# Optimization experiments

Measured on AMD Instinct MI355X. Metric: run time of the kernel, lower is better.

The kernel has to match this reference:

```python
import jax, jax.numpy as jnp
import numpy as np

B, S, P = 256, 1024, 4096   # batch, n_sensors, n_points
NM, H, PD = 64, 128, 128    # n_modes, hidden width, p
C = 1.0                     # speed of light param


def setup_inputs() -> dict:
    key = jax.random.key(0)
    ks = jax.random.split(key, 16)
    w = lambda k, shp: (jax.random.normal(k, shp, jnp.float32) * 0.05)
    return {
        "u0": jax.random.normal(ks[0], (B, S), jnp.float32),
        "x": jax.random.uniform(ks[1], (P,), jnp.float32, -1.0, 1.0),
        "t": jax.random.uniform(ks[2], (P,), jnp.float32, 0.0, 1.0),
        # branch MLP: (2*NM)->128->128->PD
        "bw1": w(ks[3], (H, 2 * NM)), "bb1": jnp.zeros((H,), jnp.float32),
        "bw2": w(ks[4], (H, H)),      "bb2": jnp.zeros((H,), jnp.float32),
        "bw3": w(ks[5], (PD, H)),     "bb3": jnp.zeros((PD,), jnp.float32),
        # trunk MLP: 4->128->128->PD
        "tw1": w(ks[6], (H, 4)),      "tb1": jnp.zeros((H,), jnp.float32),
        "tw2": w(ks[7], (H, H)),      "tb2": jnp.zeros((H,), jnp.float32),
        "tw3": w(ks[8], (PD, H)),     "tb3": jnp.zeros((PD,), jnp.float32),
    }


def _mlp(a, w1, b1, w2, b2, w3, b3):
    a = jax.nn.relu(a @ w1.T + b1)
    a = jax.nn.relu(a @ w2.T + b2)
    return a @ w3.T + b3


def reference(u0, x, t, bw1, bb1, bw2, bb2, bw3, bb3, tw1, tb1, tw2, tb2, tw3, tb3):
    # Fourier coefficients: mean over sensors of u0 * cos/sin(pi*k*xs)
    xs = jnp.linspace(-1.0, 1.0, S, dtype=jnp.float32)          # (S,)
    modes = jnp.arange(1, NM + 1, dtype=jnp.float32)            # (NM,)
    ang = jnp.pi * modes[:, None] * xs[None, :]                 # (NM, S)
    cos_c = (u0 @ jnp.cos(ang).T) / S                           # (B, NM)
    sin_c = (u0 @ jnp.sin(ang).T) / S                           # (B, NM)
    fourier = jnp.concatenate([cos_c, sin_c], axis=1)           # (B, 2*NM)

    branch_out = _mlp(fourier, bw1, bb1, bw2, bb2, bw3, bb3)    # (B, PD)

    xe = jnp.broadcast_to(x[None, :], (u0.shape[0], P))         # (B, P)
    te = jnp.broadcast_to(t[None, :], (u0.shape[0], P))
    pt_sq = te ** 2 - xe ** 2 / (C ** 2)
    # safe sqrt of clamp(pt_sq, min=0)
    proper_time = jnp.sqrt(jnp.where(pt_sq > 0, pt_sq, 0.0) + 0.0)
    causal = (jnp.abs(xe) <= C * te).astype(jnp.float32)
    trunk_feat = jnp.stack([xe, te, proper_time, causal], axis=-1)  # (B, P, 4)

    trunk_out = _mlp(trunk_feat, tw1, tb1, tw2, tb2, tw3, tb3)      # (B, P, PD)

    u_pred = jnp.einsum("bd,bpd->bp", branch_out, trunk_out)        # (B, P)
    return u_pred * causal
```

## Files before the change

### kernel.cpp

```cpp
#include <hip/hip_runtime.h>
#include <hip/hip_fp16.h>
#include <math.h>

#define NMODES 64
#define SDIM   1024
#define BATCH  256
#define PDIM   4096
#define HDIM   128

typedef _Float16 half8 __attribute__((ext_vector_type(8)));
typedef float f32x4 __attribute__((ext_vector_type(4)));

#define WSB_BRANCH 0
#define WSB_T3     (BATCH * HDIM * 2)

__global__ __launch_bounds__(256) void k_fused(
    const float* __restrict__ u0,
    const float* __restrict__ xv, const float* __restrict__ tv,
    const float* __restrict__ bw1, const float* __restrict__ bb1,
    const float* __restrict__ bw2, const float* __restrict__ bb2,
    const float* __restrict__ bw3, const float* __restrict__ bb3,
    const float* __restrict__ tw1, const float* __restrict__ tb1,
    const float* __restrict__ tw2, const float* __restrict__ tb2,
    const float* __restrict__ tw3, const float* __restrict__ tb3,
    __half* __restrict__ branch_out, __half* __restrict__ t3g) {
    __shared__ float h1L[16 * 132];
    __shared__ float h2L[16 * 132];
    __shared__ float featL[16][4];
    __shared__ float u0s[2][SDIM];
    __shared__ float part[2][2][HDIM];
    __shared__ float fr[2][HDIM];
    __shared__ float hh[2][HDIM];

    const int t = threadIdx.x;

    if (blockIdx.x < 256) {
        const int pbase = blockIdx.x * 16;
        const int j = t & 127;
        const int pg = t >> 7;

        if (t < 16) {
            int p = pbase + t;
            float x = xv[p], tt = tv[p];
            float q = tt * tt - x * x;
            float ptime = (q > 0.f) ? sqrtf(q) : 0.f;
            float c = (fabsf(x) <= tt) ? 1.f : 0.f;
            featL[t][0] = x; featL[t][1] = tt; featL[t][2] = ptime; featL[t][3] = c;
        }
        __syncthreads();

        {
            float4 w1 = ((const float4*)tw1)[j];
            float b1 = tb1[j];
            for (int p = pg; p < 16; p += 2) {
                float4 f = *(const float4*)featL[p];
                float v = fmaf(w1.x, f.x, fmaf(w1.y, f.y, fmaf(w1.z, f.z, fmaf(w1.w, f.w, b1))));
                h1L[p * 132 + j] = fmaxf(v, 0.f);
            }
        }
        __syncthreads();

        {
            const float4* wp = (const float4*)(tw2 + (size_t)j * HDIM);
            float bias = tb2[j];
            float acc[8];
#pragma unroll
            for (int q = 0; q < 8; ++q) acc[q] = bias;
            for (int i4 = 0; i4 < 32; ++i4) {
                float4 wv = wp[i4];
#pragma unroll
                for (int q = 0; q < 8; ++q) {
                    float4 hv = *(const float4*)&h1L[(pg + q * 2) * 132 + i4 * 4];
                    acc[q] += wv.x * hv.x + wv.y * hv.y + wv.z * hv.z + wv.w * hv.w;
                }
            }
#pragma unroll
            for (int q = 0; q < 8; ++q) h2L[(pg + q * 2) * 132 + j] = fmaxf(acc[q], 0.f);
        }
        __syncthreads();

        {
            const float4* wp = (const float4*)(tw3 + (size_t)j * HDIM);
            float bias = tb3[j];
            float acc[8];
#pragma unroll
            for (int q = 0; q < 8; ++q) acc[q] = bias;
            for (int i4 = 0; i4 < 32; ++i4) {
                float4 wv = wp[i4];
#pragma unroll
                for (int q = 0; q < 8; ++q) {
                    float4 hv = *(const float4*)&h2L[(pg + q * 2) * 132 + i4 * 4];
                    acc[q] += wv.x * hv.x + wv.y * hv.y + wv.z * hv.z + wv.w * hv.w;
                }
            }
#pragma unroll
            for (int q = 0; q < 8; ++q)
                t3g[(size_t)(pbase + pg + q * 2) * HDIM + j] = __float2half(acc[q]);
        }
        return;
    }

    const int bb = (blockIdx.x - 256) * 2;
    const int j = t & 127;
    const int half = t >> 7;

    {
        int flat0 = t;
        int row0 = flat0 >> 8, c40 = flat0 & 255;
        ((float4*)u0s[row0])[c40] = ((const float4*)(u0 + (size_t)(bb + row0) * SDIM))[c40];
        int flat1 = t + 256;
        int row1 = flat1 >> 8, c41 = flat1 & 255;
        ((float4*)u0s[row1])[c41] = ((const float4*)(u0 + (size_t)(bb + row1) * SDIM))[c41];
    }
    __syncthreads();

    {
        const int kmode = (j & 63) + 1;
        const int s_lo = half * 512;
        float xs0 = -1.0f + 2.0f * (float)s_lo / 1023.0f;
        float a = 0.5f * (float)kmode * xs0;
        a = a - floorf(a);
        const float r = (float)kmode * (1.0f / 1023.0f);
        float a0 = 0.f, a1 = 0.f;
        if (j < 64) {
#pragma unroll 8
            for (int s = s_lo; s < s_lo + 512; ++s) {
                float bas = __builtin_amdgcn_cosf(a);
                a += r; a = a - floorf(a);
                a0 += bas * u0s[0][s];
                a1 += bas * u0s[1][s];
            }
        } else {
#pragma unroll 8
            for (int s = s_lo; s < s_lo + 512; ++s) {
                float bas = __builtin_amdgcn_sinf(a);
                a += r; a = a - floorf(a);
                a0 += bas * u0s[0][s];
                a1 += bas * u0s[1][s];
            }
        }
        part[half][0][j] = a0;
        part[half][1][j] = a1;
    }
    __syncthreads();
    if (t < 128) {
        const float sc = 1.0f / (float)SDIM;
        fr[0][j] = (part[0][0][j] + part[1][0][j]) * sc;
        fr[1][j] = (part[0][1][j] + part[1][1][j]) * sc;
    }
    __syncthreads();

    if (t < 128) {
        {
            const float4* wp = (const float4*)(bw1 + (size_t)j * HDIM);
            float c0 = bb1[j], c1 = c0;
            for (int i4 = 0; i4 < 32; ++i4) {
                float4 wv = wp[i4];
                float4 x0 = *(const float4*)&fr[0][i4 * 4];
                float4 x1 = *(const float4*)&fr[1][i4 * 4];
                c0 += wv.x * x0.x + wv.y * x0.y + wv.z * x0.z + wv.w * x0.w;
                c1 += wv.x * x1.x + wv.y * x1.y + wv.z * x1.z + wv.w * x1.w;
            }
            hh[0][j] = fmaxf(c0, 0.f); hh[1][j] = fmaxf(c1, 0.f);
        }
        __syncthreads();
        {
            const float4* wp = (const float4*)(bw2 + (size_t)j * HDIM);
            float c0 = bb2[j], c1 = c0;
            for (int i4 = 0; i4 < 32; ++i4) {
                float4 wv = wp[i4];
                float4 x0 = *(const float4*)&hh[0][i4 * 4];
                float4 x1 = *(const float4*)&hh[1][i4 * 4];
                c0 += wv.x * x0.x + wv.y * x0.y + wv.z * x0.z + wv.w * x0.w;
                c1 += wv.x * x1.x + wv.y * x1.y + wv.z * x1.z + wv.w * x1.w;
            }
            fr[0][j] = fmaxf(c0, 0.f); fr[1][j] = fmaxf(c1, 0.f);
        }
        __syncthreads();
        {
            const float4* wp = (const float4*)(bw3 + (size_t)j * HDIM);
            float c0 = bb3[j], c1 = c0;
            for (int i4 = 0; i4 < 32; ++i4) {
                float4 wv = wp[i4];
                float4 x0 = *(const float4*)&fr[0][i4 * 4];
                float4 x1 = *(const float4*)&fr[1][i4 * 4];
                c0 += wv.x * x0.x + wv.y * x0.y + wv.z * x0.z + wv.w * x0.w;
                c1 += wv.x * x1.x + wv.y * x1.y + wv.z * x1.z + wv.w * x1.w;
            }
            branch_out[(size_t)(bb + 0) * HDIM + j] = __float2half(c0);
            branch_out[(size_t)(bb + 1) * HDIM + j] = __float2half(c1);
        }
    } else {
        __syncthreads();
        __syncthreads();
    }
}

#define LDH 144
__global__ __launch_bounds__(256) void k_final(
    const __half* __restrict__ br_g, const __half* __restrict__ t3g,
    const float* __restrict__ xv, const float* __restrict__ tv,
    float* __restrict__ out) {
    __shared__ _Float16 brL[64 * LDH];
    __shared__ _Float16 ttL[64 * LDH];
    __shared__ float causL[64];

    const int t = threadIdx.x;
    const int rb = blockIdx.x >> 6;
    const int cb = blockIdx.x & 63;

    if (t < 64) {
        int p = cb * 64 + t;
        float x = xv[p], tt = tv[p];
        causL[t] = (fabsf(x) <= tt) ? 1.f : 0.f;
    }

#pragma unroll
    for (int it = 0; it < 4; ++it) {
        int flat = t + 256 * it;
        int row = flat >> 4, c = flat & 15;
        *(float4*)&brL[row * LDH + c * 8] =
            *(const float4*)&br_g[(size_t)(rb * 64 + row) * HDIM + c * 8];
        *(float4*)&ttL[row * LDH + c * 8] =
            *(const float4*)&t3g[(size_t)(cb * 64 + row) * HDIM + c * 8];
    }
    __syncthreads();

    const int lane = t & 63;
    const int w = t >> 6;
    const int lm = lane & 15;
    const int q = lane >> 4;

    f32x4 acc[4] = {f32x4{0,0,0,0}, f32x4{0,0,0,0}, f32x4{0,0,0,0}, f32x4{0,0,0,0}};

    const _Float16* aBase = &brL[(16 * w + lm) * LDH + q * 8];
#pragma unroll
    for (int ks = 0; ks < 4; ++ks) {
        half8 af = *(const half8*)(aBase + ks * 32);
#pragma unroll
        for (int jt = 0; jt < 4; ++jt) {
            half8 bf = *(const half8*)&ttL[(16 * jt + lm) * LDH + q * 8 + ks * 32];
            acc[jt] = __builtin_amdgcn_mfma_f32_16x16x32_f16(af, bf, acc[jt], 0, 0, 0);
        }
    }

#pragma unroll
    for (int jt = 0; jt < 4; ++jt) {
        int col = cb * 64 + 16 * jt + lm;
        float cz = causL[16 * jt + lm];
#pragma unroll
        for (int e = 0; e < 4; ++e) {
            int row = rb * 64 + 16 * w + q * 4 + e;
            out[(size_t)row * PDIM + col] = acc[jt][e] * cz;
        }
    }
}

extern "C" void kernel_launch(void* const* d_in, const int* in_sizes, int n_in,
                              void* d_out, int out_size, void* d_ws, size_t ws_size,
                              hipStream_t stream) {
    const float* u0  = (const float*)d_in[0];
    const float* xv  = (const float*)d_in[1];
    const float* tv  = (const float*)d_in[2];
    const float* bw1 = (const float*)d_in[3];
    const float* bb1 = (const float*)d_in[4];
    const float* bw2 = (const float*)d_in[5];
    const float* bb2 = (const float*)d_in[6];
    const float* bw3 = (const float*)d_in[7];
    const float* bb3 = (const float*)d_in[8];
    const float* tw1 = (const float*)d_in[9];
    const float* tb1 = (const float*)d_in[10];
    const float* tw2 = (const float*)d_in[11];
    const float* tb2 = (const float*)d_in[12];
    const float* tw3 = (const float*)d_in[13];
    const float* tb3 = (const float*)d_in[14];

    char* wsb = (char*)d_ws;
    __half* branch_out = (__half*)(wsb + WSB_BRANCH);
    __half* t3g        = (__half*)(wsb + WSB_T3);
    float* out = (float*)d_out;

    hipLaunchKernelGGL(k_fused, dim3(384), dim3(256), 0, stream,
                       u0, xv, tv, bw1, bb1, bw2, bb2, bw3, bb3,
                       tw1, tb1, tw2, tb2, tw3, tb3, branch_out, t3g);
    hipLaunchKernelGGL(k_final, dim3(256), dim3(256), 0, stream,
                       branch_out, t3g, xv, tv, out);
}
```

Baseline: 107.3 us.

## Merge both kernels into one cooperative launch with grid sync and even/odd folding

Fuses the trunk/branch MLP kernel and the final MFMA contraction into a single cooperative kernel of 256 blocks, separated by a grid-wide sync, with shared memory overlaid through a union. Each block now handles 16 trunk points plus one batch row of the branch path. The Fourier projection uses the symmetry of the sensor grid, folding u0 into even and odd halves so the cos and sin loops run over half as many samples. This removes a kernel launch and gap and balances work across blocks, at the cost of a grid barrier and lower per-block parallelism in the branch MLP.

```diff
diff --git a/kernel.cpp b/kernel.cpp
--- a/kernel.cpp
+++ b/kernel.cpp
@@ -1,12 +1,16 @@
 #include <hip/hip_runtime.h>
 #include <hip/hip_fp16.h>
+#include <hip/hip_cooperative_groups.h>
 #include <math.h>
+
+namespace cg = cooperative_groups;
 
 #define NMODES 64
 #define SDIM   1024
 #define BATCH  256
 #define PDIM   4096
 #define HDIM   128
+#define LDH    144
 
 typedef _Float16 half8 __attribute__((ext_vector_type(8)));
 typedef float f32x4 __attribute__((ext_vector_type(4)));
@@ -14,7 +18,24 @@
 #define WSB_BRANCH 0
 #define WSB_T3     (BATCH * HDIM * 2)
 
-__global__ __launch_bounds__(256) void k_fused(
+struct P1 {
+    float h1L[16 * 132];
+    float h2L[16 * 132];
+    float featL[16][4];
+    float ue[512];
+    float uo[512];
+    float part[2][HDIM];
+    float fr[HDIM];
+    float hh[HDIM];
+};
+struct P2 {
+    _Float16 brL[64 * LDH];
+    _Float16 ttL[64 * LDH];
+    float causL[64];
+};
+union SharedU { P1 p1; P2 p2; };
+
+__global__ __launch_bounds__(256) void k_all(
     const float* __restrict__ u0,
     const float* __restrict__ xv, const float* __restrict__ tv,
     const float* __restrict__ bw1, const float* __restrict__ bb1,
@@ -23,29 +44,25 @@
     const float* __restrict__ tw1, const float* __restrict__ tb1,
     const float* __restrict__ tw2, const float* __restrict__ tb2,
     const float* __restrict__ tw3, const float* __restrict__ tb3,
-    __half* __restrict__ branch_out, __half* __restrict__ t3g) {
-    __shared__ float h1L[16 * 132];
-    __shared__ float h2L[16 * 132];
-    __shared__ float featL[16][4];
-    __shared__ float u0s[2][SDIM];
-    __shared__ float part[2][2][HDIM];
-    __shared__ float fr[2][HDIM];
-    __shared__ float hh[2][HDIM];
+    __half* __restrict__ branch_out, __half* __restrict__ t3g,
+    float* __restrict__ out) {
+    __shared__ SharedU sh;
 
     const int t = threadIdx.x;
-
-    if (blockIdx.x < 256) {
-        const int pbase = blockIdx.x * 16;
-        const int j = t & 127;
-        const int pg = t >> 7;
-
+    const int b = blockIdx.x;
+    const int j = t & 127;
+    const int pg = t >> 7;
+
+    {
+        const int pbase = b * 16;
         if (t < 16) {
             int p = pbase + t;
             float x = xv[p], tt = tv[p];
             float q = tt * tt - x * x;
             float ptime = (q > 0.f) ? sqrtf(q) : 0.f;
             float c = (fabsf(x) <= tt) ? 1.f : 0.f;
-            featL[t][0] = x; featL[t][1] = tt; featL[t][2] = ptime; featL[t][3] = c;
+            sh.p1.featL[t][0] = x; sh.p1.featL[t][1] = tt;
+            sh.p1.featL[t][2] = ptime; sh.p1.featL[t][3] = c;
         }
         __syncthreads();
 
@@ -53,9 +70,9 @@
             float4 w1 = ((const float4*)tw1)[j];
             float b1 = tb1[j];
             for (int p = pg; p < 16; p += 2) {
-                float4 f = *(const float4*)featL[p];
+                float4 f = *(const float4*)sh.p1.featL[p];
                 float v = fmaf(w1.x, f.x, fmaf(w1.y, f.y, fmaf(w1.z, f.z, fmaf(w1.w, f.w, b1))));
-                h1L[p * 132 + j] = fmaxf(v, 0.f);
+                sh.p1.h1L[p * 132 + j] = fmaxf(v, 0.f);
             }
         }
         __syncthreads();
@@ -70,12 +87,12 @@
                 float4 wv = wp[i4];
 #pragma unroll
                 for (int q = 0; q < 8; ++q) {
-                    float4 hv = *(const float4*)&h1L[(pg + q * 2) * 132 + i4 * 4];
+                    float4 hv = *(const float4*)&sh.p1.h1L[(pg + q * 2) * 132 + i4 * 4];
                     acc[q] += wv.x * hv.x + wv.y * hv.y + wv.z * hv.z + wv.w * hv.w;
                 }
             }
 #pragma unroll
-            for (int q = 0; q < 8; ++q) h2L[(pg + q * 2) * 132 + j] = fmaxf(acc[q], 0.f);
+            for (int q = 0; q < 8; ++q) sh.p1.h2L[(pg + q * 2) * 132 + j] = fmaxf(acc[q], 0.f);
         }
         __syncthreads();
 
@@ -89,7 +106,7 @@
                 float4 wv = wp[i4];
 #pragma unroll
                 for (int q = 0; q < 8; ++q) {
-                    float4 hv = *(const float4*)&h2L[(pg + q * 2) * 132 + i4 * 4];
+                    float4 hv = *(const float4*)&sh.p1.h2L[(pg + q * 2) * 132 + i4 * 4];
                     acc[q] += wv.x * hv.x + wv.y * hv.y + wv.z * hv.z + wv.w * hv.w;
                 }
             }
@@ -97,161 +114,136 @@
             for (int q = 0; q < 8; ++q)
                 t3g[(size_t)(pbase + pg + q * 2) * HDIM + j] = __float2half(acc[q]);
         }
-        return;
-    }
-
-    const int bb = (blockIdx.x - 256) * 2;
-    const int j = t & 127;
-    const int half = t >> 7;
-
-    {
-        int flat0 = t;
-        int row0 = flat0 >> 8, c40 = flat0 & 255;
-        ((float4*)u0s[row0])[c40] = ((const float4*)(u0 + (size_t)(bb + row0) * SDIM))[c40];
-        int flat1 = t + 256;
-        int row1 = flat1 >> 8, c41 = flat1 & 255;
-        ((float4*)u0s[row1])[c41] = ((const float4*)(u0 + (size_t)(bb + row1) * SDIM))[c41];
     }
     __syncthreads();
 
     {
-        const int kmode = (j & 63) + 1;
-        const int s_lo = half * 512;
-        float xs0 = -1.0f + 2.0f * (float)s_lo / 1023.0f;
-        float a = 0.5f * (float)kmode * xs0;
-        a = a - floorf(a);
-        const float r = (float)kmode * (1.0f / 1023.0f);
-        float a0 = 0.f, a1 = 0.f;
-        if (j < 64) {
+        const float* up = u0 + (size_t)b * SDIM;
+        for (int s = t; s < 512; s += 256) {
+            float a = up[s];
+            float c = up[1023 - s];
+            sh.p1.ue[s] = a + c;
+            sh.p1.uo[s] = a - c;
+        }
+        __syncthreads();
+
+        {
+            const int kmode = (j & 63) + 1;
+            const int s_lo = pg * 256;
+            float a = 0.5f * (float)kmode * (-1.0f + 2.0f * (float)s_lo / 1023.0f);
+            a -= floorf(a);
+            const float r = (float)kmode * (1.0f / 1023.0f);
+            float acc = 0.f;
+            if (j < 64) {
 #pragma unroll 8
-            for (int s = s_lo; s < s_lo + 512; ++s) {
-                float bas = __builtin_amdgcn_cosf(a);
-                a += r; a = a - floorf(a);
-                a0 += bas * u0s[0][s];
-                a1 += bas * u0s[1][s];
-            }
-        } else {
+                for (int s = s_lo; s < s_lo + 256; ++s) {
+                    float bas = __builtin_amdgcn_cosf(a);
+                    a += r; a -= floorf(a);
+                    acc += bas * sh.p1.ue[s];
+                }
+            } else {
 #pragma unroll 8
-            for (int s = s_lo; s < s_lo + 512; ++s) {
-                float bas = __builtin_amdgcn_sinf(a);
-                a += r; a = a - floorf(a);
-                a0 += bas * u0s[0][s];
-                a1 += bas * u0s[1][s];
-            }
-        }
-        part[half][0][j] = a0;
-        part[half][1][j] = a1;
+                for (int s = s_lo; s < s_lo + 256; ++s) {
+                    float bas = __builtin_amdgcn_sinf(a);
+                    a += r; a -= floorf(a);
+                    acc += bas * sh.p1.uo[s];
+                }
+            }
+            sh.p1.part[pg][j] = acc;
+        }
+        __syncthreads();
+        if (t < 128)
+            sh.p1.fr[j] = (sh.p1.part[0][j] + sh.p1.part[1][j]) * (1.0f / (float)SDIM);
+        __syncthreads();
+
+        float c0 = 0.f;
+        if (t < 128) {
+            const float4* wp = (const float4*)(bw1 + (size_t)j * HDIM);
+            c0 = bb1[j];
+            for (int i4 = 0; i4 < 32; ++i4) {
+                float4 wv = wp[i4];
+                float4 x0 = *(const float4*)&sh.p1.fr[i4 * 4];
+                c0 += wv.x * x0.x + wv.y * x0.y + wv.z * x0.z + wv.w * x0.w;
+            }
+        }
+        __syncthreads();
+        if (t < 128) sh.p1.hh[j] = fmaxf(c0, 0.f);
+        __syncthreads();
+        if (t < 128) {
+            const float4* wp = (const float4*)(bw2 + (size_t)j * HDIM);
+            c0 = bb2[j];
+            for (int i4 = 0; i4 < 32; ++i4) {
+                float4 wv = wp[i4];
+                float4 x0 = *(const float4*)&sh.p1.hh[i4 * 4];
+                c0 += wv.x * x0.x + wv.y * x0.y + wv.z * x0.z + wv.w * x0.w;
+            }
+        }
+        __syncthreads();
+        if (t < 128) sh.p1.fr[j] = fmaxf(c0, 0.f);
+        __syncthreads();
+        if (t < 128) {
+            const float4* wp = (const float4*)(bw3 + (size_t)j * HDIM);
+            c0 = bb3[j];
+            for (int i4 = 0; i4 < 32; ++i4) {
+                float4 wv = wp[i4];
+                float4 x0 = *(const float4*)&sh.p1.fr[i4 * 4];
+                c0 += wv.x * x0.x + wv.y * x0.y + wv.z * x0.z + wv.w * x0.w;
+            }
+            branch_out[(size_t)b * HDIM + j] = __float2half(c0);
+        }
     }
-    __syncthreads();
-    if (t < 128) {
-        const float sc = 1.0f / (float)SDIM;
-        fr[0][j] = (part[0][0][j] + part[1][0][j]) * sc;
-        fr[1][j] = (part[0][1][j] + part[1][1][j]) * sc;
-    }
-    __syncthreads();
-
-    if (t < 128) {
-        {
-            const float4* wp = (const float4*)(bw1 + (size_t)j * HDIM);
-            float c0 = bb1[j], c1 = c0;
-            for (int i4 = 0; i4 < 32; ++i4) {
-                float4 wv = wp[i4];
-                float4 x0 = *(const float4*)&fr[0][i4 * 4];
-                float4 x1 = *(const float4*)&fr[1][i4 * 4];
-                c0 += wv.x * x0.x + wv.y * x0.y + wv.z * x0.z + wv.w * x0.w;
-                c1 += wv.x * x1.x + wv.y * x1.y + wv.z * x1.z + wv.w * x1.w;
-            }
-            hh[0][j] = fmaxf(c0, 0.f); hh[1][j] = fmaxf(c1, 0.f);
-        }
-        __syncthreads();
-        {
-            const float4* wp = (const float4*)(bw2 + (size_t)j * HDIM);
-            float c0 = bb2[j], c1 = c0;
-            for (int i4 = 0; i4 < 32; ++i4) {
-                float4 wv = wp[i4];
-                float4 x0 = *(const float4*)&hh[0][i4 * 4];
-                float4 x1 = *(const float4*)&hh[1][i4 * 4];
-                c0 += wv.x * x0.x + wv.y * x0.y + wv.z * x0.z + wv.w * x0.w;
-                c1 += wv.x * x1.x + wv.y * x1.y + wv.z * x1.z + wv.w * x1.w;
-            }
-            fr[0][j] = fmaxf(c0, 0.f); fr[1][j] = fmaxf(c1, 0.f);
-        }
-        __syncthreads();
-        {
-            const float4* wp = (const float4*)(bw3 + (size_t)j * HDIM);
-            float c0 = bb3[j], c1 = c0;
-            for (int i4 = 0; i4 < 32; ++i4) {
-                float4 wv = wp[i4];
-                float4 x0 = *(const float4*)&fr[0][i4 * 4];
-                float4 x1 = *(const float4*)&fr[1][i4 * 4];
-                c0 += wv.x * x0.x + wv.y * x0.y + wv.z * x0.z + wv.w * x0.w;
-                c1 += wv.x * x1.x + wv.y * x1.y + wv.z * x1.z + wv.w * x1.w;
-            }
-            branch_out[(size_t)(bb + 0) * HDIM + j] = __float2half(c0);
-            branch_out[(size_t)(bb + 1) * HDIM + j] = __float2half(c1);
-        }
-    } else {
-        __syncthreads();
-        __syncthreads();
-    }
-}
-
-#define LDH 144
-__global__ __launch_bounds__(256) void k_final(
-    const __half* __restrict__ br_g, const __half* __restrict__ t3g,
-    const float* __restrict__ xv, const float* __restrict__ tv,
-    float* __restrict__ out) {
-    __shared__ _Float16 brL[64 * LDH];
-    __shared__ _Float16 ttL[64 * LDH];
-    __shared__ float causL[64];
-
-    const int t = threadIdx.x;
-    const int rb = blockIdx.x >> 6;
-    const int cb = blockIdx.x & 63;
-
-    if (t < 64) {
-        int p = cb * 64 + t;
-        float x = xv[p], tt = tv[p];
-        causL[t] = (fabsf(x) <= tt) ? 1.f : 0.f;
-    }
-
-#pragma unroll
-    for (int it = 0; it < 4; ++it) {
-        int flat = t + 256 * it;
-        int row = flat >> 4, c = flat & 15;
-        *(float4*)&brL[row * LDH + c * 8] =
-            *(const float4*)&br_g[(size_t)(rb * 64 + row) * HDIM + c * 8];
-        *(float4*)&ttL[row * LDH + c * 8] =
-            *(const float4*)&t3g[(size_t)(cb * 64 + row) * HDIM + c * 8];
-    }
-    __syncthreads();
-
-    const int lane = t & 63;
-    const int w = t >> 6;
-    const int lm = lane & 15;
-    const int q = lane >> 4;
-
-    f32x4 acc[4] = {f32x4{0,0,0,0}, f32x4{0,0,0,0}, f32x4{0,0,0,0}, f32x4{0,0,0,0}};
-
-    const _Float16* aBase = &brL[(16 * w + lm) * LDH + q * 8];
-#pragma unroll
-    for (int ks = 0; ks < 4; ++ks) {
-        half8 af = *(const half8*)(aBase + ks * 32);
+
+    __threadfence();
+    cg::this_grid().sync();
+
+    {
+        const int rb = b >> 6;
+        const int cb = b & 63;
+
+        if (t < 64) {
+            int p = cb * 64 + t;
+            float x = xv[p], tt = tv[p];
+            sh.p2.causL[t] = (fabsf(x) <= tt) ? 1.f : 0.f;
+        }
+
+#pragma unroll
+        for (int it = 0; it < 4; ++it) {
+            int flat = t + 256 * it;
+            int row = flat >> 4, c = flat & 15;
+            *(float4*)&sh.p2.brL[row * LDH + c * 8] =
+                *(const float4*)&branch_out[(size_t)(rb * 64 + row) * HDIM + c * 8];
+            *(float4*)&sh.p2.ttL[row * LDH + c * 8] =
+                *(const float4*)&t3g[(size_t)(cb * 64 + row) * HDIM + c * 8];
+        }
+        __syncthreads();
+
+        const int lane = t & 63;
+        const int w = t >> 6;
+        const int lm = lane & 15;
+        const int q = lane >> 4;
+
+        f32x4 acc[4] = {f32x4{0,0,0,0}, f32x4{0,0,0,0}, f32x4{0,0,0,0}, f32x4{0,0,0,0}};
+
+        const _Float16* aBase = &sh.p2.brL[(16 * w + lm) * LDH + q * 8];
+#pragma unroll
+        for (int ks = 0; ks < 4; ++ks) {
+            half8 af = *(const half8*)(aBase + ks * 32);
+#pragma unroll
+            for (int jt = 0; jt < 4; ++jt) {
+                half8 bf = *(const half8*)&sh.p2.ttL[(16 * jt + lm) * LDH + q * 8 + ks * 32];
+                acc[jt] = __builtin_amdgcn_mfma_f32_16x16x32_f16(af, bf, acc[jt], 0, 0, 0);
+            }
+        }
+
 #pragma unroll
         for (int jt = 0; jt < 4; ++jt) {
-            half8 bf = *(const half8*)&ttL[(16 * jt + lm) * LDH + q * 8 + ks * 32];
-            acc[jt] = __builtin_amdgcn_mfma_f32_16x16x32_f16(af, bf, acc[jt], 0, 0, 0);
-        }
-    }
-
-#pragma unroll
-    for (int jt = 0; jt < 4; ++jt) {
-        int col = cb * 64 + 16 * jt + lm;
-        float cz = causL[16 * jt + lm];
-#pragma unroll
-        for (int e = 0; e < 4; ++e) {
-            int row = rb * 64 + 16 * w + q * 4 + e;
-            out[(size_t)row * PDIM + col] = acc[jt][e] * cz;
+            int col = cb * 64 + 16 * jt + lm;
+            float cz = sh.p2.causL[16 * jt + lm];
+#pragma unroll
+            for (int e = 0; e < 4; ++e) {
+                int row = rb * 64 + 16 * w + q * 4 + e;
+                out[(size_t)row * PDIM + col] = acc[jt][e] * cz;
+            }
         }
     }
 }
@@ -280,9 +272,14 @@
     __half* t3g        = (__half*)(wsb + WSB_T3);
     float* out = (float*)d_out;
 
-    hipLaunchKernelGGL(k_fused, dim3(384), dim3(256), 0, stream,
-                       u0, xv, tv, bw1, bb1, bw2, bb2, bw3, bb3,
-                       tw1, tb1, tw2, tb2, tw3, tb3, branch_out, t3g);
-    hipLaunchKernelGGL(k_final, dim3(256), dim3(256), 0, stream,
-                       branch_out, t3g, xv, tv, out);
+    void* args[] = {
+        (void*)&u0, (void*)&xv, (void*)&tv,
+        (void*)&bw1, (void*)&bb1, (void*)&bw2, (void*)&bb2,
+        (void*)&bw3, (void*)&bb3,
+        (void*)&tw1, (void*)&tb1, (void*)&tw2, (void*)&tb2,
+        (void*)&tw3, (void*)&tb3,
+        (void*)&branch_out, (void*)&t3g, (void*)&out,
+    };
+    hipLaunchCooperativeKernel((const void*)k_all, dim3(256), dim3(256),
+                               args, 0, stream);
 }
```

New measurement: 177.8 us. +65.7%, slower.

## Exploit cos/sin sensor symmetry and register-block trunk MLP over two output units

Applied to the files above, without the earlier changes.

Sensor grid xs is symmetric, so cos terms pair with u0[s]+u0[1023-s] and sin terms with u0[s]-u0[1023-s]. Folding the inputs this way halves the Fourier loop length per thread. Separately, the trunk hidden and output layers now give each thread two output units over four points, so each h-tile LDS read is reused for two weight rows. The costs are a strided reversed global read during folding and a different per-thread register footprint.

```diff
diff --git a/kernel.cpp b/kernel.cpp
--- a/kernel.cpp
+++ b/kernel.cpp
@@ -27,7 +27,8 @@
     __shared__ float h1L[16 * 132];
     __shared__ float h2L[16 * 132];
     __shared__ float featL[16][4];
-    __shared__ float u0s[2][SDIM];
+    __shared__ float ue[2][512];
+    __shared__ float uo[2][512];
     __shared__ float part[2][2][HDIM];
     __shared__ float fr[2][HDIM];
     __shared__ float hh[2][HDIM];
@@ -60,42 +61,57 @@
         }
         __syncthreads();
 
-        {
-            const float4* wp = (const float4*)(tw2 + (size_t)j * HDIM);
-            float bias = tb2[j];
-            float acc[8];
-#pragma unroll
-            for (int q = 0; q < 8; ++q) acc[q] = bias;
-            for (int i4 = 0; i4 < 32; ++i4) {
-                float4 wv = wp[i4];
-#pragma unroll
-                for (int q = 0; q < 8; ++q) {
-                    float4 hv = *(const float4*)&h1L[(pg + q * 2) * 132 + i4 * 4];
-                    acc[q] += wv.x * hv.x + wv.y * hv.y + wv.z * hv.z + wv.w * hv.w;
+        const int u2 = t & 63;
+        const int pq = t >> 6;
+
+        {
+            const float4* wpA = (const float4*)(tw2 + (size_t)u2 * HDIM);
+            const float4* wpB = (const float4*)(tw2 + (size_t)(u2 + 64) * HDIM);
+            float accA[4], accB[4];
+            float ba = tb2[u2], bbv = tb2[u2 + 64];
+#pragma unroll
+            for (int n = 0; n < 4; ++n) { accA[n] = ba; accB[n] = bbv; }
+            for (int i4 = 0; i4 < 32; ++i4) {
+                float4 wa = wpA[i4];
+                float4 wb = wpB[i4];
+#pragma unroll
+                for (int n = 0; n < 4; ++n) {
+                    float4 x4 = *(const float4*)&h1L[(pq + 4 * n) * 132 + i4 * 4];
+                    accA[n] += wa.x * x4.x + wa.y * x4.y + wa.z * x4.z + wa.w * x4.w;
+                    accB[n] += wb.x * x4.x + wb.y * x4.y + wb.z * x4.z + wb.w * x4.w;
                 }
             }
 #pragma unroll
-            for (int q = 0; q < 8; ++q) h2L[(pg + q * 2) * 132 + j] = fmaxf(acc[q], 0.f);
-        }
-        __syncthreads();
-
-        {
-            const float4* wp = (const float4*)(tw3 + (size_t)j * HDIM);
-            float bias = tb3[j];
-            float acc[8];
-#pragma unroll
-            for (int q = 0; q < 8; ++q) acc[q] = bias;
-            for (int i4 = 0; i4 < 32; ++i4) {
-                float4 wv = wp[i4];
-#pragma unroll
-                for (int q = 0; q < 8; ++q) {
-                    float4 hv = *(const float4*)&h2L[(pg + q * 2) * 132 + i4 * 4];
-                    acc[q] += wv.x * hv.x + wv.y * hv.y + wv.z * hv.z + wv.w * hv.w;
+            for (int n = 0; n < 4; ++n) {
+                h2L[(pq + 4 * n) * 132 + u2]      = fmaxf(accA[n], 0.f);
+                h2L[(pq + 4 * n) * 132 + u2 + 64] = fmaxf(accB[n], 0.f);
+            }
+        }
+        __syncthreads();
+
+        {
+            const float4* wpA = (const float4*)(tw3 + (size_t)u2 * HDIM);
+            const float4* wpB = (const float4*)(tw3 + (size_t)(u2 + 64) * HDIM);
+            float accA[4], accB[4];
+            float ba = tb3[u2], bbv = tb3[u2 + 64];
+#pragma unroll
+            for (int n = 0; n < 4; ++n) { accA[n] = ba; accB[n] = bbv; }
+            for (int i4 = 0; i4 < 32; ++i4) {
+                float4 wa = wpA[i4];
+                float4 wb = wpB[i4];
+#pragma unroll
+                for (int n = 0; n < 4; ++n) {
+                    float4 x4 = *(const float4*)&h2L[(pq + 4 * n) * 132 + i4 * 4];
+                    accA[n] += wa.x * x4.x + wa.y * x4.y + wa.z * x4.z + wa.w * x4.w;
+                    accB[n] += wb.x * x4.x + wb.y * x4.y + wb.z * x4.z + wb.w * x4.w;
                 }
             }
 #pragma unroll
-            for (int q = 0; q < 8; ++q)
-                t3g[(size_t)(pbase + pg + q * 2) * HDIM + j] = __float2half(acc[q]);
+            for (int n = 0; n < 4; ++n) {
+                size_t row = (size_t)(pbase + pq + 4 * n) * HDIM;
+                t3g[row + u2]      = __float2half(accA[n]);
+                t3g[row + u2 + 64] = __float2half(accB[n]);
+            }
         }
         return;
     }
@@ -105,38 +121,39 @@
     const int half = t >> 7;
 
     {
-        int flat0 = t;
-        int row0 = flat0 >> 8, c40 = flat0 & 255;
-        ((float4*)u0s[row0])[c40] = ((const float4*)(u0 + (size_t)(bb + row0) * SDIM))[c40];
-        int flat1 = t + 256;
-        int row1 = flat1 >> 8, c41 = flat1 & 255;
-        ((float4*)u0s[row1])[c41] = ((const float4*)(u0 + (size_t)(bb + row1) * SDIM))[c41];
+        const float* u0p = u0 + (size_t)bb * SDIM;
+        const float* u1p = u0p + SDIM;
+        for (int s = t; s < 512; s += 256) {
+            float a0 = u0p[s], c0 = u0p[1023 - s];
+            float a1 = u1p[s], c1 = u1p[1023 - s];
+            ue[0][s] = a0 + c0; uo[0][s] = a0 - c0;
+            ue[1][s] = a1 + c1; uo[1][s] = a1 - c1;
+        }
     }
     __syncthreads();
 
     {
         const int kmode = (j & 63) + 1;
-        const int s_lo = half * 512;
-        float xs0 = -1.0f + 2.0f * (float)s_lo / 1023.0f;
-        float a = 0.5f * (float)kmode * xs0;
-        a = a - floorf(a);
+        const int s_lo = half * 256;
+        float a = 0.5f * (float)kmode * (-1.0f + 2.0f * (float)s_lo / 1023.0f);
+        a -= floorf(a);
         const float r = (float)kmode * (1.0f / 1023.0f);
         float a0 = 0.f, a1 = 0.f;
         if (j < 64) {
 #pragma unroll 8
-            for (int s = s_lo; s < s_lo + 512; ++s) {
+            for (int s = s_lo; s < s_lo + 256; ++s) {
                 float bas = __builtin_amdgcn_cosf(a);
-                a += r; a = a - floorf(a);
-                a0 += bas * u0s[0][s];
-                a1 += bas * u0s[1][s];
+                a += r; a -= floorf(a);
+                a0 += bas * ue[0][s];
+                a1 += bas * ue[1][s];
             }
         } else {
 #pragma unroll 8
-            for (int s = s_lo; s < s_lo + 512; ++s) {
+            for (int s = s_lo; s < s_lo + 256; ++s) {
                 float bas = __builtin_amdgcn_sinf(a);
-                a += r; a = a - floorf(a);
-                a0 += bas * u0s[0][s];
-                a1 += bas * u0s[1][s];
+                a += r; a -= floorf(a);
+                a0 += bas * uo[0][s];
+                a1 += bas * uo[1][s];
             }
         }
         part[half][0][j] = a0;
```

After: 108.6 us. About the same (+1.1%).
